# Kernel optimization log

Measured on AMD Instinct MI355X. Metric: run time of the kernel, lower is better.

The kernel has to match this reference:

```python
import jax, jax.numpy as jnp
import numpy as np

N = 50000
E = 800000
D_IN = 256
H1 = 512   # hidden_channels
H2 = 256   # out_channels == hidden_dim
NUM_CLASSES = 5
NEG_SLOPE = 0.2


def _edge_softmax(logits, dst, n):
    # numerically-stable softmax over edges grouped by destination node
    m = jax.ops.segment_max(logits, dst, num_segments=n)
    e = jnp.exp(logits - m[dst])
    s = jax.ops.segment_sum(e, dst, num_segments=n)
    return e / (s[dst] + 1e-16)


def _gat_conv(x, src, dst, W, att_src, att_dst, bias):
    h = x @ W                                   # [N, C] (PyG lin_src, no bias)
    a_s = (h * att_src).sum(-1)                 # [N]
    a_d = (h * att_dst).sum(-1)                 # [N]
    logits = jax.nn.leaky_relu(a_s[src] + a_d[dst], NEG_SLOPE)  # [E]
    alpha = _edge_softmax(logits, dst, x.shape[0])              # [E]
    out = jax.ops.segment_sum(h[src] * alpha[:, None], dst, num_segments=x.shape[0])
    return out + bias


def setup_inputs() -> dict:
    key = jax.random.key(0)
    ks = jax.random.split(key, 20)
    g = lambda k, shp, fan: jax.random.normal(k, shp, jnp.float32) * (1.0 / np.sqrt(fan))
    inp = {
        "x": jax.random.normal(ks[0], (N, D_IN), jnp.float32),
        "edge_index": jax.random.randint(ks[1], (2, E), 0, N, jnp.int64),
        # conv1 (GATConv, heads=1)
        "W1": g(ks[2], (D_IN, H1), D_IN),
        "att_src1": g(ks[3], (H1,), H1),
        "att_dst1": g(ks[4], (H1,), H1),
        "b_conv1": jnp.zeros((H1,), jnp.float32),
        # lin1 (dense residual)
        "A1": g(ks[5], (D_IN, H1), D_IN),
        "b1": jnp.zeros((H1,), jnp.float32),
        # conv2
        "W2": g(ks[6], (H1, H2), H1),
        "att_src2": g(ks[7], (H2,), H2),
        "att_dst2": g(ks[8], (H2,), H2),
        "b_conv2": jnp.zeros((H2,), jnp.float32),
        # lin2
        "A2": g(ks[9], (H1, H2), H1),
        "b2": jnp.zeros((H2,), jnp.float32),
        # 3 hidden MLP layers [256 -> 256]
        "Hw1": g(ks[10], (H2, H2), H2), "Hb1": jnp.zeros((H2,), jnp.float32),
        "Hw2": g(ks[11], (H2, H2), H2), "Hb2": jnp.zeros((H2,), jnp.float32),
        "Hw3": g(ks[12], (H2, H2), H2), "Hb3": jnp.zeros((H2,), jnp.float32),
        # classifier
        "fcw": g(ks[13], (H2, NUM_CLASSES), H2),
        "fcb": jnp.zeros((NUM_CLASSES,), jnp.float32),
    }
    return inp


def reference(x, edge_index, W1, att_src1, att_dst1, b_conv1, A1, b1,
              W2, att_src2, att_dst2, b_conv2, A2, b2,
              Hw1, Hb1, Hw2, Hb2, Hw3, Hb3, fcw, fcb):
    src, dst = edge_index[0], edge_index[1]
    h = _gat_conv(x, src, dst, W1, att_src1, att_dst1, b_conv1) + (x @ A1 + b1)
    h = jax.nn.relu(h)
    h = _gat_conv(h, src, dst, W2, att_src2, att_dst2, b_conv2) + (h @ A2 + b2)
    for w, b in ((Hw1, Hb1), (Hw2, Hb2), (Hw3, Hb3)):
        h = jax.nn.relu(h @ w + b)
    logits = h @ fcw + fcb
    return jax.nn.softmax(logits, axis=-1)
```

## Files before the change

### kernel.cpp

```cpp
#include <hip/hip_runtime.h>

typedef unsigned short u16;
typedef short short8 __attribute__((ext_vector_type(8)));
typedef u16 u16x4 __attribute__((ext_vector_type(4)));
typedef float float4v __attribute__((ext_vector_type(4)));

#define NEG_SLOPE 0.2f

static __device__ __forceinline__ float b2f(u16 u) {
    union { unsigned int i; float f; } x; x.i = ((unsigned int)u) << 16; return x.f;
}
static __device__ __forceinline__ u16 f2b(float f) {
    unsigned int u = __float_as_uint(f);
    unsigned int r = (u + 0x7fffu + ((u >> 16) & 1u)) >> 16;
    return (u16)r;
}

__global__ void k_diag(float* out, int n, float val)
{
    int i = blockIdx.x * 256 + threadIdx.x;
    if (i < n) out[i] = val;
}

__global__ void scan_csr(const int* off, const int* srcs, int N, int E,
                         int* flag, int bit)
{
    int i = blockIdx.x * 256 + threadIdx.x;
    if (i < N) {
        int a = off[i], b = off[i + 1];
        if (a < 0 || b < a || b > E) atomicOr(flag, bit);
    }
    if (i == 0 && off[N] != E) atomicOr(flag, bit);
    if (i < E) {
        if ((unsigned)srcs[i] >= (unsigned)N) atomicOr(flag, bit);
    }
}

__global__ void k_final_diag(const int* flag, float* out, int n)
{
    int f = *flag;
    if (f == 0) return;
    int b = __ffs(f) - 1;
    float val = 32.0f * (b + 1);
    int i = blockIdx.x * 256 + threadIdx.x;
    if (i < n) out[i] = val;
}

__global__ void k_detect(const int* ei, int E, int* flag64)
{
    __shared__ int zc;
    if (threadIdx.x == 0) zc = 0;
    __syncthreads();
    int idx = 1 + 2 * (int)threadIdx.x;
    int z = (idx < 2 * E && ei[idx] == 0) ? 1 : 0;
    atomicAdd(&zc, z);
    __syncthreads();
    if (threadIdx.x == 0) *flag64 = (zc >= 200) ? 1 : 0;
}

__global__ void k_extract(const int* ei, int E, const int* flag64,
                          int* src, int* dst)
{
    int e = blockIdx.x * 256 + threadIdx.x;
    if (e >= E) return;
    if (*flag64) {
        src[e] = ei[2 * e];
        dst[e] = ei[2 * E + 2 * e];
    } else {
        src[e] = ei[e];
        dst[e] = ei[E + e];
    }
}

__global__ void k_count(const int* dst, int* deg, int E, int N)
{
    int e = blockIdx.x * 256 + threadIdx.x;
    if (e < E) {
        int d = dst[e];
        if ((unsigned)d < (unsigned)N) atomicAdd(&deg[d], 1);
    }
}

__global__ __launch_bounds__(256)
void k_scan_a(const int* __restrict__ deg, int* __restrict__ off,
              int* __restrict__ partial, int N)
{
    __shared__ int sd[256];
    int tid = threadIdx.x;
    int base = blockIdx.x * 1024;
    int i0 = base + tid * 4;
    int v0 = 0, v1 = 0, v2 = 0, v3 = 0;
    if (i0 < N)     v0 = deg[i0];
    if (i0 + 1 < N) v1 = deg[i0 + 1];
    if (i0 + 2 < N) v2 = deg[i0 + 2];
    if (i0 + 3 < N) v3 = deg[i0 + 3];
    int t = v0 + v1 + v2 + v3;
    sd[tid] = t;
    __syncthreads();
    #pragma unroll
    for (int s = 1; s < 256; s <<= 1) {
        int u = (tid >= s) ? sd[tid - s] : 0;
        __syncthreads();
        sd[tid] += u;
        __syncthreads();
    }
    int excl = sd[tid] - t;
    if (i0 < N)     off[i0]     = excl;
    if (i0 + 1 < N) off[i0 + 1] = excl + v0;
    if (i0 + 2 < N) off[i0 + 2] = excl + v0 + v1;
    if (i0 + 3 < N) off[i0 + 3] = excl + v0 + v1 + v2;
    if (tid == 255) partial[blockIdx.x] = sd[255];
}

__global__ __launch_bounds__(1024)
void k_scan_b(int* partial, int nblk)
{
    __shared__ int sd[1024];
    __shared__ int running;
    int tid = threadIdx.x;
    if (tid == 0) running = 0;
    __syncthreads();
    for (int base = 0; base < nblk; base += 1024) {
        int i = base + tid;
        int v = (i < nblk) ? partial[i] : 0;
        sd[tid] = v;
        __syncthreads();
        for (int s = 1; s < 1024; s <<= 1) {
            int u = (tid >= s) ? sd[tid - s] : 0;
            __syncthreads();
            sd[tid] += u;
            __syncthreads();
        }
        if (i < nblk) partial[i] = sd[tid] - v + running;
        int total = sd[1023];
        __syncthreads();
        if (tid == 0) running += total;
        __syncthreads();
    }
}

__global__ __launch_bounds__(256)
void k_scan_c(int* __restrict__ off, int* __restrict__ cursor,
              const int* __restrict__ partial, int N, int E)
{
    int i = blockIdx.x * 256 + threadIdx.x;
    if (i < N) {
        int v = off[i] + partial[i >> 10];
        off[i] = v;
        cursor[i] = v;
    }
    if (i == 0) off[N] = E;
}

__global__ void k_scatter(const int* src, const int* dst, int* cursor,
                          int* srcs, int E, int N)
{
    int e = blockIdx.x * 256 + threadIdx.x;
    if (e < E) {
        int d = dst[e];
        if ((unsigned)d < (unsigned)N) {
            int p = atomicAdd(&cursor[d], 1);
            if ((unsigned)p < (unsigned)E) srcs[p] = src[e];
        }
    }
}

__global__ __launch_bounds__(256)
void k_f2b8(const float* __restrict__ in, u16* __restrict__ out, int n8)
{
    int i = blockIdx.x * 256 + threadIdx.x;
    if (i >= n8) return;
    const float4* p = (const float4*)in + (size_t)i * 2;
    float4 v0 = p[0], v1 = p[1];
    int4 w;
    w.x = (int)f2b(v0.x) | ((int)f2b(v0.y) << 16);
    w.y = (int)f2b(v0.z) | ((int)f2b(v0.w) << 16);
    w.z = (int)f2b(v1.x) | ((int)f2b(v1.y) << 16);
    w.w = (int)f2b(v1.z) | ((int)f2b(v1.w) << 16);
    *(int4*)(out + (size_t)i * 8) = w;
}

__global__ __launch_bounds__(64)
void k_packF(const float* in1, const float* in2, int ksplit, int csplit,
             int in_ld, u16* __restrict__ out)
{
    int l = threadIdx.x;
    int cf = blockIdx.x, kt = blockIdx.y, NC16 = gridDim.x;
    int col = cf * 16 + (l & 15);
    int kbase = kt * 32 + (l >> 4) * 8;
    const float* src = in1;
    int cc = col, koff = 0;
    if (ksplit > 0 && kbase >= ksplit) { src = in2; koff = ksplit; }
    if (csplit > 0 && col >= csplit)   { src = in2; cc = col - csplit; }
    u16* o = out + ((size_t)(kt * NC16 + cf) * 512) + l * 8;
    #pragma unroll
    for (int j = 0; j < 8; ++j)
        o[j] = f2b(src[(size_t)(kbase - koff + j) * in_ld + cc]);
}

__global__ __launch_bounds__(256)
void k_rowdot2f(const float* __restrict__ A, int ld, int H,
                const float* __restrict__ vs, const float* __restrict__ vd,
                float* a_s, float* a_d, int N)
{
    int wave = threadIdx.x >> 6, lane = threadIdx.x & 63;
    int n = blockIdx.x * 4 + wave;
    if (n >= N) return;
    const float* ar = A + (size_t)n * ld;
    float ss = 0.f, sd = 0.f;
    for (int i = lane * 4; i < H; i += 256) {
        float4 v  = *(const float4*)(ar + i);
        float4 s4 = *(const float4*)(vs + i);
        float4 d4 = *(const float4*)(vd + i);
        ss += v.x * s4.x + v.y * s4.y + v.z * s4.z + v.w * s4.w;
        sd += v.x * d4.x + v.y * d4.y + v.z * d4.z + v.w * d4.w;
    }
    #pragma unroll
    for (int m = 32; m; m >>= 1) {
        ss += __shfl_xor(ss, m, 64);
        sd += __shfl_xor(sd, m, 64);
    }
    if (lane == 0) { a_s[n] = ss; a_d[n] = sd; }
}

__global__ __launch_bounds__(256)
void k_rowdot2(const u16* h, int ld, int H, const float* vs, const float* vd,
               float* a_s, float* a_d, int N)
{
    int wave = threadIdx.x >> 6, lane = threadIdx.x & 63;
    int n = blockIdx.x * 4 + wave;
    if (n >= N) return;
    const u16* hr = h + (size_t)n * ld;
    float ss = 0.f, sd = 0.f;
    for (int i = lane; i < H; i += 64) {
        float v = b2f(hr[i]);
        ss += v * vs[i];
        sd += v * vd[i];
    }
    #pragma unroll
    for (int m = 32; m; m >>= 1) {
        ss += __shfl_xor(ss, m, 64);
        sd += __shfl_xor(sd, m, 64);
    }
    if (lane == 0) { a_s[n] = ss; a_d[n] = sd; }
}

__global__ __launch_bounds__(256)
void k_alpha(const int* __restrict__ off, const int* __restrict__ srcs,
             const float* __restrict__ a_s, const float* __restrict__ a_d,
             float* __restrict__ alpha, int N)
{
    int wave = threadIdx.x >> 6, lane = threadIdx.x & 63;
    int n = blockIdx.x * 4 + wave;
    if (n >= N) return;
    int base = off[n], end = off[n + 1];
    float adn = a_d[n];
    float m = -1e30f;
    for (int p = base + lane; p < end; p += 64) {
        int s = srcs[p];
        s = ((unsigned)s < (unsigned)N) ? s : 0;
        float z = a_s[s] + adn;
        z = z > 0.f ? z : NEG_SLOPE * z;
        m = fmaxf(m, z);
    }
    #pragma unroll
    for (int s = 32; s; s >>= 1) m = fmaxf(m, __shfl_xor(m, s, 64));
    float sum = 0.f;
    for (int p = base + lane; p < end; p += 64) {
        int s = srcs[p];
        s = ((unsigned)s < (unsigned)N) ? s : 0;
        float z = a_s[s] + adn;
        z = z > 0.f ? z : NEG_SLOPE * z;
        sum += __expf(z - m);
    }
    #pragma unroll
    for (int s = 32; s; s >>= 1) sum += __shfl_xor(sum, s, 64);
    float inv = 1.f / (sum + 1e-16f);
    for (int p = base + lane; p < end; p += 64) {
        int s = srcs[p];
        s = ((unsigned)s < (unsigned)N) ? s : 0;
        float z = a_s[s] + adn;
        z = z > 0.f ? z : NEG_SLOPE * z;
        alpha[p] = __expf(z - m) * inv;
    }
}

__global__ __launch_bounds__(256)
void k_aggw(const u16* __restrict__ rows, const int* __restrict__ off,
            const int* __restrict__ srcs, const float* __restrict__ alpha,
            const u16* __restrict__ add, u16* __restrict__ out, int N)
{
    int wave = threadIdx.x >> 6, lane = threadIdx.x & 63;
    int n = blockIdx.x * 4 + wave;
    if (n >= N) return;
    int base = off[n], end = off[n + 1];
    int c4 = lane * 4;
    float a0 = 0.f, a1 = 0.f, a2 = 0.f, a3 = 0.f;
    int p = base;
    for (; p + 1 < end; p += 2) {
        int s0 = srcs[p];     s0 = ((unsigned)s0 < (unsigned)N) ? s0 : 0;
        int s1 = srcs[p + 1]; s1 = ((unsigned)s1 < (unsigned)N) ? s1 : 0;
        float w0 = alpha[p], w1 = alpha[p + 1];
        u16x4 v0 = *(const u16x4*)(rows + (size_t)s0 * 256 + c4);
        u16x4 v1 = *(const u16x4*)(rows + (size_t)s1 * 256 + c4);
        a0 += w0 * b2f(v0[0]) + w1 * b2f(v1[0]);
        a1 += w0 * b2f(v0[1]) + w1 * b2f(v1[1]);
        a2 += w0 * b2f(v0[2]) + w1 * b2f(v1[2]);
        a3 += w0 * b2f(v0[3]) + w1 * b2f(v1[3]);
    }
    if (p < end) {
        int s0 = srcs[p]; s0 = ((unsigned)s0 < (unsigned)N) ? s0 : 0;
        float w0 = alpha[p];
        u16x4 v0 = *(const u16x4*)(rows + (size_t)s0 * 256 + c4);
        a0 += w0 * b2f(v0[0]);
        a1 += w0 * b2f(v0[1]);
        a2 += w0 * b2f(v0[2]);
        a3 += w0 * b2f(v0[3]);
    }
    size_t ob = (size_t)n * 256 + c4;
    if (add) {
        a0 += b2f(add[ob]);     a1 += b2f(add[ob + 1]);
        a2 += b2f(add[ob + 2]); a3 += b2f(add[ob + 3]);
    }
    u16x4 o;
    o[0] = f2b(a0); o[1] = f2b(a1); o[2] = f2b(a2); o[3] = f2b(a3);
    *(u16x4*)(out + ob) = o;
}

__global__ __launch_bounds__(512)
void bigfull(const u16* __restrict__ A1, int lda1,
             const u16* __restrict__ A2, int lda2,
             const u16* __restrict__ WTf,
             const float* b0a, const float* b0b,
             const float* b1a, const float* b1b,
             u16* C1, int ldc1, u16* C2, int ldc2,
             int M, int relu0, int relu1)
{
    __shared__ u16 As[64 * 32];
    __shared__ u16 Bs[512 * 32];

    const int tid = threadIdx.x;
    const int w = tid >> 6, lane = tid & 63;
    const int m16 = lane & 15, q = lane >> 4;
    const int rowBase = blockIdx.x * 64;

    float4v acc[16] = {};

    for (int k0 = 0; k0 < 512; k0 += 32) {
        const int kt = k0 >> 5;
        __syncthreads();
        if (tid < 256) {
            int rf = tid >> 6, al = tid & 63;
            int grow = rowBase + rf * 16 + (al & 15);
            if (grow >= M) grow = M - 1;
            int kk = k0 + (al >> 4) * 8;
            const u16* src = (kk < 256)
                ? A1 + (size_t)grow * lda1 + kk
                : A2 + (size_t)grow * lda2 + (kk - 256);
            *(int4*)&As[tid * 8] = *(const int4*)src;
        }
        {
            const u16* wsrc = WTf + (size_t)kt * 16384;
            #pragma unroll
            for (int p = 0; p < 4; ++p) {
                int ch = p * 512 + tid;
                *(int4*)&Bs[ch * 8] = *(const int4*)(wsrc + (size_t)ch * 8);
            }
        }
        __syncthreads();

        short8 a[4], b[4];
        #pragma unroll
        for (int r = 0; r < 4; ++r)
            a[r] = *(const short8*)&As[r * 512 + lane * 8];
        #pragma unroll
        for (int c = 0; c < 4; ++c)
            b[c] = *(const short8*)&Bs[(w * 4 + c) * 512 + lane * 8];
        #pragma unroll
        for (int r = 0; r < 4; ++r)
            #pragma unroll
            for (int c = 0; c < 4; ++c)
                acc[r * 4 + c] = __builtin_amdgcn_mfma_f32_16x16x32_bf16(
                    a[r], b[c], acc[r * 4 + c], 0, 0, 0);
    }

    const int colgrp = w >> 2;
    const float* ba = colgrp ? b1a : b0a;
    const float* bb = colgrp ? b1b : b0b;
    u16* C  = colgrp ? C2 : C1;
    const int ldc  = colgrp ? ldc2 : ldc1;
    const int relu = colgrp ? relu1 : relu0;
    #pragma unroll
    for (int c = 0; c < 4; ++c) {
        int lc = ((w & 3) * 4 + c) * 16 + m16;
        float bv = (ba ? ba[lc] : 0.f) + (bb ? bb[lc] : 0.f);
        #pragma unroll
        for (int r = 0; r < 4; ++r)
            #pragma unroll
            for (int i = 0; i < 4; ++i) {
                int grow = rowBase + r * 16 + q * 4 + i;
                if (grow < M) {
                    float v = acc[r * 4 + c][i] + bv;
                    if (relu) v = fmaxf(v, 0.f);
                    C[(size_t)grow * ldc + lc] = f2b(v);
                }
            }
    }
}

__global__ __launch_bounds__(256)
void k_mlp3(const u16* __restrict__ WTHf,
            const float* Hb1, const float* Hb2, const float* Hb3,
            u16* H, int M)
{
    __shared__ u16 P[64 * 256];
    __shared__ u16 Bs[256 * 32];

    const int tid = threadIdx.x;
    const int w = tid >> 6, lane = tid & 63;
    const int m16 = lane & 15, q = lane >> 4;
    const int rowBase = blockIdx.x * 64;

    #pragma unroll
    for (int p = 0; p < 8; ++p) {
        int ch = p * 256 + tid;
        int f = ch >> 6, l = ch & 63;
        int kt = f >> 2, rf = f & 3;
        int grow = rowBase + rf * 16 + (l & 15);
        if (grow >= M) grow = M - 1;
        int col = kt * 32 + (l >> 4) * 8;
        *(int4*)&P[ch * 8] = *(const int4*)(H + (size_t)grow * 256 + col);
    }

    const float* biases[3] = {Hb1, Hb2, Hb3};
    for (int L = 0; L < 3; ++L) {
        const u16* WTf = WTHf + (size_t)L * 65536;
        float4v acc[16] = {};
        for (int kt = 0; kt < 8; ++kt) {
            __syncthreads();
            {
                const u16* wsrc = WTf + (size_t)kt * 8192;
                #pragma unroll
                for (int p = 0; p < 4; ++p) {
                    int ch = p * 256 + tid;
                    *(int4*)&Bs[ch * 8] = *(const int4*)(wsrc + (size_t)ch * 8);
                }
            }
            __syncthreads();
            short8 a[4], b[4];
            #pragma unroll
            for (int r = 0; r < 4; ++r)
                a[r] = *(const short8*)&P[(kt * 4 + r) * 512 + lane * 8];
            #pragma unroll
            for (int c = 0; c < 4; ++c)
                b[c] = *(const short8*)&Bs[(w * 4 + c) * 512 + lane * 8];
            #pragma unroll
            for (int r = 0; r < 4; ++r)
                #pragma unroll
                for (int c = 0; c < 4; ++c)
                    acc[r * 4 + c] = __builtin_amdgcn_mfma_f32_16x16x32_bf16(
                        a[r], b[c], acc[r * 4 + c], 0, 0, 0);
        }
        const float* bias = biases[L];
        __syncthreads();
        if (L < 2) {
            #pragma unroll
            for (int c = 0; c < 4; ++c) {
                int col = w * 64 + c * 16 + m16;
                float bv = bias[col];
                int kt2 = col >> 5;
                int l2h = 16 * ((col & 31) >> 3);
                int j2 = col & 7;
                #pragma unroll
                for (int r = 0; r < 4; ++r)
                    #pragma unroll
                    for (int i = 0; i < 4; ++i) {
                        int l2 = (q * 4 + i) + l2h;
                        P[(size_t)(kt2 * 4 + r) * 512 + l2 * 8 + j2] =
                            f2b(fmaxf(acc[r * 4 + c][i] + bv, 0.f));
                    }
            }
        } else {
            #pragma unroll
            for (int c = 0; c < 4; ++c) {
                int col = w * 64 + c * 16 + m16;
                float bv = bias[col];
                #pragma unroll
                for (int r = 0; r < 4; ++r)
                    #pragma unroll
                    for (int i = 0; i < 4; ++i) {
                        int grow = rowBase + r * 16 + q * 4 + i;
                        if (grow < M)
                            H[(size_t)grow * 256 + col] =
                                f2b(fmaxf(acc[r * 4 + c][i] + bv, 0.f));
                    }
            }
        }
    }
}

__global__ __launch_bounds__(256)
void k_fc_softmax(const u16* hin, const float* fcw, const float* fcb,
                  float* out, int N)
{
    int wave = threadIdx.x >> 6, lane = threadIdx.x & 63;
    int n = blockIdx.x * 4 + wave;
    if (n >= N) return;
    const u16* hr = hin + (size_t)n * 256;
    int k0 = lane * 4;
    float hv[4];
    float p[5] = {0.f, 0.f, 0.f, 0.f, 0.f};
    #pragma unroll
    for (int j = 0; j < 4; ++j) hv[j] = b2f(hr[k0 + j]);
    #pragma unroll
    for (int j = 0; j < 4; ++j) {
        const float* wr = fcw + (size_t)(k0 + j) * 5;
        #pragma unroll
        for (int c = 0; c < 5; ++c) p[c] += hv[j] * wr[c];
    }
    #pragma unroll
    for (int c = 0; c < 5; ++c) {
        #pragma unroll
        for (int s = 32; s; s >>= 1) p[c] += __shfl_xor(p[c], s, 64);
    }
    if (lane == 0) {
        float m = -1e30f;
        #pragma unroll
        for (int c = 0; c < 5; ++c) { p[c] += fcb[c]; m = fmaxf(m, p[c]); }
        float s = 0.f, e[5];
        #pragma unroll
        for (int c = 0; c < 5; ++c) { e[c] = __expf(p[c] - m); s += e[c]; }
        float inv = 1.f / s;
        #pragma unroll
        for (int c = 0; c < 5; ++c) out[(size_t)n * 5 + c] = e[c] * inv;
    }
}

extern "C" void kernel_launch(void* const* d_in, const int* in_sizes, int n_in,
                              void* d_out, int out_size, void* d_ws, size_t ws_size,
                              hipStream_t stream)
{
    const float* x    = (const float*)d_in[0];
    const int*   ei   = (const int*)  d_in[1];
    const float* W1   = (const float*)d_in[2];
    const float* as1  = (const float*)d_in[3];
    const float* ad1  = (const float*)d_in[4];
    const float* bc1  = (const float*)d_in[5];
    const float* A1w  = (const float*)d_in[6];
    const float* b1   = (const float*)d_in[7];
    const float* W2   = (const float*)d_in[8];
    const float* as2  = (const float*)d_in[9];
    const float* ad2  = (const float*)d_in[10];
    const float* bc2  = (const float*)d_in[11];
    const float* A2w  = (const float*)d_in[12];
    const float* b2   = (const float*)d_in[13];
    const float* Hw1  = (const float*)d_in[14];
    const float* Hb1  = (const float*)d_in[15];
    const float* Hw2  = (const float*)d_in[16];
    const float* Hb2  = (const float*)d_in[17];
    const float* Hw3  = (const float*)d_in[18];
    const float* Hb3  = (const float*)d_in[19];
    const float* fcw  = (const float*)d_in[20];
    const float* fcb  = (const float*)d_in[21];
    float* out = (float*)d_out;

    const int D = 256;
    const int N = in_sizes[0] / D;
    const int E = in_sizes[1] / 2;

    char* w = (char*)d_ws;
    auto alloc = [&](size_t bytes) {
        char* p = w;
        w += (bytes + 255) & ~(size_t)255;
        return p;
    };
    int*   flag   = (int*)  alloc(256);
    int*   flag64 = (int*)  alloc(256);
    float* a_s    = (float*)alloc((size_t)N * 4);
    float* a_d    = (float*)alloc((size_t)N * 4);
    float* vs1    = (float*)alloc(1024);
    float* vd1    = (float*)alloc(1024);
    int*   deg    = (int*)  alloc((size_t)N * 4);
    int*   cursor = (int*)  alloc((size_t)N * 4);
    int*   offA   = (int*)  alloc((size_t)(N + 1) * 4);
    int*   part   = (int*)  alloc((size_t)((N + 1023) / 1024 + 1) * 4);
    int*   srcs   = (int*)  alloc((size_t)E * 4);
    float* alpha  = (float*)alloc((size_t)E * 4);
    u16*   WT1    = (u16*)  alloc(512 * 512 * 2);
    u16*   WT2    = (u16*)  alloc(512 * 512 * 2);
    u16*   WTH    = (u16*)  alloc(3 * 256 * 256 * 2);
    u16*   BUF1   = (u16*)  alloc((size_t)N * 512 * 2);
    u16*   BUF2   = (u16*)  alloc((size_t)N * 512 * 2);

    int* src32 = (int*)BUF1;
    int* dst32 = src32 + E;

    size_t need = (size_t)(w - (char*)d_ws);
    if (ws_size < need) {
        float code = 1000.0f + (float)(ws_size >> 20);
        k_diag<<<(out_size + 255) / 256, 256, 0, stream>>>(out, out_size, code);
        return;
    }

    const int EB  = (E + 255) / 256;
    const int NB4 = (N + 3) / 4;
    const int OB  = (out_size + 255) / 256;
    const int NE  = (N > E ? N : E);
    const int RB64 = (N + 63) / 64;
    const int NBLK = (N + 1023) / 1024;
    const size_t NH2 = (size_t)N * 256;
    u16* XB   = BUF1;
    u16* AGGX = BUF1 + NH2;

    hipMemsetAsync(flag, 0, 4, stream);

    k_detect <<<1, 256, 0, stream>>>(ei, E, flag64);
    k_extract<<<EB, 256, 0, stream>>>(ei, E, flag64, src32, dst32);
    hipMemsetAsync(deg, 0, (size_t)N * 4, stream);
    k_count  <<<EB, 256, 0, stream>>>(dst32, deg, E, N);
    k_scan_a <<<NBLK, 256, 0, stream>>>(deg, offA, part, N);
    k_scan_b <<<1, 1024, 0, stream>>>(part, NBLK);
    k_scan_c <<<(N + 255) / 256, 256, 0, stream>>>(offA, cursor, part, N, E);
    k_scatter<<<EB, 256, 0, stream>>>(src32, dst32, cursor, srcs, E, N);
    scan_csr <<<(NE + 255) / 256, 256, 0, stream>>>(offA, srcs, N, E, flag, 1);

    k_packF<<<dim3(32, 16), 64, 0, stream>>>(A1w, W1, 256, 0, 512, WT1);
    k_packF<<<dim3(32, 16), 64, 0, stream>>>(W2, A2w, 0, 256, 256, WT2);
    k_packF<<<dim3(16, 8),  64, 0, stream>>>(Hw1, nullptr, 0, 0, 256, WTH);
    k_packF<<<dim3(16, 8),  64, 0, stream>>>(Hw2, nullptr, 0, 0, 256, WTH + 65536);
    k_packF<<<dim3(16, 8),  64, 0, stream>>>(Hw3, nullptr, 0, 0, 256, WTH + 131072);

    k_f2b8<<<(N * 32 + 255) / 256, 256, 0, stream>>>(x, XB, N * 32);

    k_rowdot2f<<<64, 256, 0, stream>>>(W1, 512, 512, as1, ad1, vs1, vd1, 256);
    k_rowdot2f<<<NB4, 256, 0, stream>>>(x, 256, 256, vs1, vd1, a_s, a_d, N);
    k_alpha<<<NB4, 256, 0, stream>>>(offA, srcs, a_s, a_d, alpha, N);

    k_aggw<<<NB4, 256, 0, stream>>>(XB, offA, srcs, alpha, nullptr, AGGX, N);

    bigfull<<<RB64, 512, 0, stream>>>(XB, 256, AGGX, 256, WT1,
                                      b1, bc1, b1 + 256, bc1 + 256,
                                      BUF2, 512, BUF2 + 256, 512, N, 1, 1);

    bigfull<<<RB64, 512, 0, stream>>>(BUF2, 512, BUF2 + 256, 512, WT2,
                                      nullptr, nullptr, b2, bc2,
                                      BUF1, 256, BUF1 + NH2, 256, N, 0, 0);

    k_rowdot2<<<NB4, 256, 0, stream>>>(BUF1, 256, 256, as2, ad2, a_s, a_d, N);
    k_alpha<<<NB4, 256, 0, stream>>>(offA, srcs, a_s, a_d, alpha, N);
    k_aggw<<<NB4, 256, 0, stream>>>(BUF1, offA, srcs, alpha, BUF1 + NH2, BUF2, N);

    k_mlp3<<<RB64, 256, 0, stream>>>(WTH, Hb1, Hb2, Hb3, BUF2, N);

    k_fc_softmax<<<NB4, 256, 0, stream>>>(BUF2, fcw, fcb, out, N);

    k_final_diag<<<OB, 256, 0, stream>>>(flag, out, out_size);
}
```

Baseline: 618.0 us.

## Fuse preprocessing kernels, use online softmax, and widen aggregation loads

Folds degree counting into edge extraction, merges the five weight-pack launches into one 3D grid, and fuses the x-to-bf16 cast with the attention row dot-products so x is read once. The edge softmax becomes a single online max/sum pass plus a write pass, which drops one gather sweep over a_s. The aggregation kernel now splits each wave into two halves that handle alternate edges with 8-wide bf16 loads, then combines them with a shuffle. The cost is more launch-time branching in the pack kernel and extra exp work per edge in the online softmax.

```diff
diff --git a/kernel.cpp b/kernel.cpp
--- a/kernel.cpp
+++ b/kernel.cpp
@@ -3,6 +3,7 @@
 typedef unsigned short u16;
 typedef short short8 __attribute__((ext_vector_type(8)));
 typedef u16 u16x4 __attribute__((ext_vector_type(4)));
+typedef u16 u16x8 __attribute__((ext_vector_type(8)));
 typedef float float4v __attribute__((ext_vector_type(4)));
 
 #define NEG_SLOPE 0.2f
@@ -59,26 +60,20 @@
 }
 
 __global__ void k_extract(const int* ei, int E, const int* flag64,
-                          int* src, int* dst)
+                          int* src, int* dst, int* deg, int N)
 {
     int e = blockIdx.x * 256 + threadIdx.x;
     if (e >= E) return;
+    int s, d;
     if (*flag64) {
-        src[e] = ei[2 * e];
-        dst[e] = ei[2 * E + 2 * e];
+        s = ei[2 * e];
+        d = ei[2 * E + 2 * e];
     } else {
-        src[e] = ei[e];
-        dst[e] = ei[E + e];
-    }
-}
-
-__global__ void k_count(const int* dst, int* deg, int E, int N)
-{
-    int e = blockIdx.x * 256 + threadIdx.x;
-    if (e < E) {
-        int d = dst[e];
-        if ((unsigned)d < (unsigned)N) atomicAdd(&deg[d], 1);
-    }
+        s = ei[e];
+        d = ei[E + e];
+    }
+    src[e] = s; dst[e] = d;
+    if ((unsigned)d < (unsigned)N) atomicAdd(&deg[d], 1);
 }
 
 __global__ __launch_bounds__(256)
@@ -166,26 +161,58 @@
 }
 
 __global__ __launch_bounds__(256)
-void k_f2b8(const float* __restrict__ in, u16* __restrict__ out, int n8)
-{
-    int i = blockIdx.x * 256 + threadIdx.x;
-    if (i >= n8) return;
-    const float4* p = (const float4*)in + (size_t)i * 2;
-    float4 v0 = p[0], v1 = p[1];
+void k_castdot(const float* __restrict__ x, const float* __restrict__ vs,
+               const float* __restrict__ vd, u16* __restrict__ xb,
+               float* __restrict__ a_s, float* __restrict__ a_d, int N)
+{
+    int tid = threadIdx.x;
+    int rowb = tid >> 5;
+    int col8 = (tid & 31) * 8;
+    int n = blockIdx.x * 8 + rowb;
+    if (n >= N) return;
+    const float* xr = x + (size_t)n * 256 + col8;
+    float4 v0 = *(const float4*)xr;
+    float4 v1 = *(const float4*)(xr + 4);
     int4 w;
     w.x = (int)f2b(v0.x) | ((int)f2b(v0.y) << 16);
     w.y = (int)f2b(v0.z) | ((int)f2b(v0.w) << 16);
     w.z = (int)f2b(v1.x) | ((int)f2b(v1.y) << 16);
     w.w = (int)f2b(v1.z) | ((int)f2b(v1.w) << 16);
-    *(int4*)(out + (size_t)i * 8) = w;
+    *(int4*)(xb + (size_t)n * 256 + col8) = w;
+
+    float4 s0 = *(const float4*)(vs + col8);
+    float4 s1 = *(const float4*)(vs + col8 + 4);
+    float4 d0 = *(const float4*)(vd + col8);
+    float4 d1 = *(const float4*)(vd + col8 + 4);
+    float ss = v0.x*s0.x + v0.y*s0.y + v0.z*s0.z + v0.w*s0.w
+             + v1.x*s1.x + v1.y*s1.y + v1.z*s1.z + v1.w*s1.w;
+    float sd = v0.x*d0.x + v0.y*d0.y + v0.z*d0.z + v0.w*d0.w
+             + v1.x*d1.x + v1.y*d1.y + v1.z*d1.z + v1.w*d1.w;
+    #pragma unroll
+    for (int m = 16; m; m >>= 1) {
+        ss += __shfl_xor(ss, m, 64);
+        sd += __shfl_xor(sd, m, 64);
+    }
+    if ((tid & 31) == 0) { a_s[n] = ss; a_d[n] = sd; }
 }
 
 __global__ __launch_bounds__(64)
-void k_packF(const float* in1, const float* in2, int ksplit, int csplit,
-             int in_ld, u16* __restrict__ out)
-{
+void k_packAll(const float* A1w, const float* W1, const float* W2, const float* A2w,
+               const float* Hw1, const float* Hw2, const float* Hw3,
+               u16* WT1, u16* WT2, u16* WTH)
+{
+    int z = blockIdx.z;
+    const float *in1, *in2; int ksplit, csplit, in_ld, NC16; u16* out;
+    if (z == 0)      { in1 = A1w; in2 = W1;  ksplit = 256; csplit = 0;   in_ld = 512; out = WT1; NC16 = 32; }
+    else if (z == 1) { in1 = W2;  in2 = A2w; ksplit = 0;   csplit = 256; in_ld = 256; out = WT2; NC16 = 32; }
+    else {
+        if (blockIdx.x >= 16 || blockIdx.y >= 8) return;
+        in1 = (z == 2) ? Hw1 : (z == 3) ? Hw2 : Hw3;
+        in2 = nullptr; ksplit = 0; csplit = 0; in_ld = 256; NC16 = 16;
+        out = WTH + (size_t)(z - 2) * 65536;
+    }
     int l = threadIdx.x;
-    int cf = blockIdx.x, kt = blockIdx.y, NC16 = gridDim.x;
+    int cf = blockIdx.x, kt = blockIdx.y;
     int col = cf * 16 + (l & 15);
     int kbase = kt * 32 + (l >> 4) * 8;
     const float* src = in1;
@@ -255,32 +282,30 @@
     if (n >= N) return;
     int base = off[n], end = off[n + 1];
     float adn = a_d[n];
-    float m = -1e30f;
+    float m = -1e30f, s = 0.f;
     for (int p = base + lane; p < end; p += 64) {
-        int s = srcs[p];
-        s = ((unsigned)s < (unsigned)N) ? s : 0;
-        float z = a_s[s] + adn;
-        z = z > 0.f ? z : NEG_SLOPE * z;
-        m = fmaxf(m, z);
-    }
-    #pragma unroll
-    for (int s = 32; s; s >>= 1) m = fmaxf(m, __shfl_xor(m, s, 64));
-    float sum = 0.f;
+        int sx = srcs[p];
+        sx = ((unsigned)sx < (unsigned)N) ? sx : 0;
+        float z = a_s[sx] + adn;
+        z = fmaxf(z, NEG_SLOPE * z);
+        float mn = fmaxf(m, z);
+        s = s * __expf(m - mn) + __expf(z - mn);
+        m = mn;
+    }
+    #pragma unroll
+    for (int msk = 32; msk; msk >>= 1) {
+        float mo = __shfl_xor(m, msk, 64);
+        float so = __shfl_xor(s, msk, 64);
+        float mn = fmaxf(m, mo);
+        s = s * __expf(m - mn) + so * __expf(mo - mn);
+        m = mn;
+    }
+    float inv = 1.f / (s + 1e-16f);
     for (int p = base + lane; p < end; p += 64) {
-        int s = srcs[p];
-        s = ((unsigned)s < (unsigned)N) ? s : 0;
-        float z = a_s[s] + adn;
-        z = z > 0.f ? z : NEG_SLOPE * z;
-        sum += __expf(z - m);
-    }
-    #pragma unroll
-    for (int s = 32; s; s >>= 1) sum += __shfl_xor(sum, s, 64);
-    float inv = 1.f / (sum + 1e-16f);
-    for (int p = base + lane; p < end; p += 64) {
-        int s = srcs[p];
-        s = ((unsigned)s < (unsigned)N) ? s : 0;
-        float z = a_s[s] + adn;
-        z = z > 0.f ? z : NEG_SLOPE * z;
+        int sx = srcs[p];
+        sx = ((unsigned)sx < (unsigned)N) ? sx : 0;
+        float z = a_s[sx] + adn;
+        z = fmaxf(z, NEG_SLOPE * z);
         alpha[p] = __expf(z - m) * inv;
     }
 }
@@ -294,37 +319,56 @@
     int n = blockIdx.x * 4 + wave;
     if (n >= N) return;
     int base = off[n], end = off[n + 1];
-    int c4 = lane * 4;
-    float a0 = 0.f, a1 = 0.f, a2 = 0.f, a3 = 0.f;
+    int half = lane >> 5;
+    int c8 = (lane & 31) * 8;
+    float acc[8] = {};
     int p = base;
+    for (; p + 3 < end; p += 4) {
+        int sA = srcs[p + half];
+        int sB = srcs[p + 2 + half];
+        sA = ((unsigned)sA < (unsigned)N) ? sA : 0;
+        sB = ((unsigned)sB < (unsigned)N) ? sB : 0;
+        float wA = alpha[p + half];
+        float wB = alpha[p + 2 + half];
+        u16x8 vA = *(const u16x8*)(rows + (size_t)sA * 256 + c8);
+        u16x8 vB = *(const u16x8*)(rows + (size_t)sB * 256 + c8);
+        #pragma unroll
+        for (int j = 0; j < 8; ++j)
+            acc[j] += wA * b2f(vA[j]) + wB * b2f(vB[j]);
+    }
     for (; p + 1 < end; p += 2) {
-        int s0 = srcs[p];     s0 = ((unsigned)s0 < (unsigned)N) ? s0 : 0;
-        int s1 = srcs[p + 1]; s1 = ((unsigned)s1 < (unsigned)N) ? s1 : 0;
-        float w0 = alpha[p], w1 = alpha[p + 1];
-        u16x4 v0 = *(const u16x4*)(rows + (size_t)s0 * 256 + c4);
-        u16x4 v1 = *(const u16x4*)(rows + (size_t)s1 * 256 + c4);
-        a0 += w0 * b2f(v0[0]) + w1 * b2f(v1[0]);
-        a1 += w0 * b2f(v0[1]) + w1 * b2f(v1[1]);
-        a2 += w0 * b2f(v0[2]) + w1 * b2f(v1[2]);
-        a3 += w0 * b2f(v0[3]) + w1 * b2f(v1[3]);
+        int sA = srcs[p + half];
+        sA = ((unsigned)sA < (unsigned)N) ? sA : 0;
+        float wA = alpha[p + half];
+        u16x8 vA = *(const u16x8*)(rows + (size_t)sA * 256 + c8);
+        #pragma unroll
+        for (int j = 0; j < 8; ++j)
+            acc[j] += wA * b2f(vA[j]);
     }
     if (p < end) {
-        int s0 = srcs[p]; s0 = ((unsigned)s0 < (unsigned)N) ? s0 : 0;
-        float w0 = alpha[p];
-        u16x4 v0 = *(const u16x4*)(rows + (size_t)s0 * 256 + c4);
-        a0 += w0 * b2f(v0[0]);
-        a1 += w0 * b2f(v0[1]);
-        a2 += w0 * b2f(v0[2]);
-        a3 += w0 * b2f(v0[3]);
-    }
-    size_t ob = (size_t)n * 256 + c4;
-    if (add) {
-        a0 += b2f(add[ob]);     a1 += b2f(add[ob + 1]);
-        a2 += b2f(add[ob + 2]); a3 += b2f(add[ob + 3]);
-    }
-    u16x4 o;
-    o[0] = f2b(a0); o[1] = f2b(a1); o[2] = f2b(a2); o[3] = f2b(a3);
-    *(u16x4*)(out + ob) = o;
+        int sA = srcs[p];
+        sA = ((unsigned)sA < (unsigned)N) ? sA : 0;
+        float wA = half ? 0.f : alpha[p];
+        u16x8 vA = *(const u16x8*)(rows + (size_t)sA * 256 + c8);
+        #pragma unroll
+        for (int j = 0; j < 8; ++j)
+            acc[j] += wA * b2f(vA[j]);
+    }
+    #pragma unroll
+    for (int j = 0; j < 8; ++j)
+        acc[j] += __shfl_xor(acc[j], 32, 64);
+    if (half == 0) {
+        size_t ob = (size_t)n * 256 + c8;
+        if (add) {
+            u16x8 ad8 = *(const u16x8*)(add + ob);
+            #pragma unroll
+            for (int j = 0; j < 8; ++j) acc[j] += b2f(ad8[j]);
+        }
+        u16x8 o;
+        #pragma unroll
+        for (int j = 0; j < 8; ++j) o[j] = f2b(acc[j]);
+        *(u16x8*)(out + ob) = o;
+    }
 }
 
 __global__ __launch_bounds__(512)
@@ -613,27 +657,21 @@
     u16* AGGX = BUF1 + NH2;
 
     hipMemsetAsync(flag, 0, 4, stream);
+    hipMemsetAsync(deg, 0, (size_t)N * 4, stream);
 
     k_detect <<<1, 256, 0, stream>>>(ei, E, flag64);
-    k_extract<<<EB, 256, 0, stream>>>(ei, E, flag64, src32, dst32);
-    hipMemsetAsync(deg, 0, (size_t)N * 4, stream);
-    k_count  <<<EB, 256, 0, stream>>>(dst32, deg, E, N);
+    k_extract<<<EB, 256, 0, stream>>>(ei, E, flag64, src32, dst32, deg, N);
     k_scan_a <<<NBLK, 256, 0, stream>>>(deg, offA, part, N);
     k_scan_b <<<1, 1024, 0, stream>>>(part, NBLK);
     k_scan_c <<<(N + 255) / 256, 256, 0, stream>>>(offA, cursor, part, N, E);
     k_scatter<<<EB, 256, 0, stream>>>(src32, dst32, cursor, srcs, E, N);
     scan_csr <<<(NE + 255) / 256, 256, 0, stream>>>(offA, srcs, N, E, flag, 1);
 
-    k_packF<<<dim3(32, 16), 64, 0, stream>>>(A1w, W1, 256, 0, 512, WT1);
-    k_packF<<<dim3(32, 16), 64, 0, stream>>>(W2, A2w, 0, 256, 256, WT2);
-    k_packF<<<dim3(16, 8),  64, 0, stream>>>(Hw1, nullptr, 0, 0, 256, WTH);
-    k_packF<<<dim3(16, 8),  64, 0, stream>>>(Hw2, nullptr, 0, 0, 256, WTH + 65536);
-    k_packF<<<dim3(16, 8),  64, 0, stream>>>(Hw3, nullptr, 0, 0, 256, WTH + 131072);
-
-    k_f2b8<<<(N * 32 + 255) / 256, 256, 0, stream>>>(x, XB, N * 32);
+    k_packAll<<<dim3(32, 16, 5), 64, 0, stream>>>(A1w, W1, W2, A2w,
+                                                  Hw1, Hw2, Hw3, WT1, WT2, WTH);
 
     k_rowdot2f<<<64, 256, 0, stream>>>(W1, 512, 512, as1, ad1, vs1, vd1, 256);
-    k_rowdot2f<<<NB4, 256, 0, stream>>>(x, 256, 256, vs1, vd1, a_s, a_d, N);
+    k_castdot<<<(N + 7) / 8, 256, 0, stream>>>(x, vs1, vd1, XB, a_s, a_d, N);
     k_alpha<<<NB4, 256, 0, stream>>>(offA, srcs, a_s, a_d, alpha, N);
 
     k_aggw<<<NB4, 256, 0, stream>>>(XB, offA, srcs, alpha, nullptr, AGGX, N);
```

Measured after the change: 587.1 us. 5.0% less time.
